# Kernel tuning notes

Measured on AMD Instinct MI355X. Metric: run time of the kernel, lower is better.

## Reference

```python
import jax, jax.numpy as jnp
import numpy as np

NINP = 768
HEAD = 12
ATTN_DIM = 768
PROT_DIM = 1024
B, T, S = 4, 2048, 512
EPS = 1e-5


def _lin_params(key, d_in, d_out):
    k1, k2 = jax.random.split(key)
    lim = 1.0 / np.sqrt(d_in)
    W = jax.random.uniform(k1, (d_in, d_out), jnp.float32, -lim, lim)
    b = jax.random.uniform(k2, (d_out,), jnp.float32, -lim, lim)
    return W, b


def setup_inputs() -> dict:
    key = jax.random.key(0)
    ks = jax.random.split(key, 16)
    x = jax.random.normal(ks[0], (B, T, NINP), jnp.float32)
    enc = jax.random.normal(ks[1], (B, S, PROT_DIM), jnp.float32)
    sWq, sbq = _lin_params(ks[2], NINP, ATTN_DIM)
    sWk, sbk = _lin_params(ks[3], NINP, ATTN_DIM)
    sWv, sbv = _lin_params(ks[4], NINP, ATTN_DIM)
    sWo, sbo = _lin_params(ks[5], ATTN_DIM, NINP)
    cWq, cbq = _lin_params(ks[6], NINP, ATTN_DIM)
    cWk, cbk = _lin_params(ks[7], PROT_DIM, ATTN_DIM)
    cWv, cbv = _lin_params(ks[8], PROT_DIM, ATTN_DIM)
    cWo, cbo = _lin_params(ks[9], ATTN_DIM, NINP)
    mW1, mb1 = _lin_params(ks[10], NINP, 4 * NINP)
    mW2, mb2 = _lin_params(ks[11], 4 * NINP, NINP)
    return dict(
        x=x, encoder_hidden_states=enc,
        ln1_g=jnp.ones((NINP,)), ln1_b=jnp.zeros((NINP,)),
        ln2_g=jnp.ones((NINP,)), ln2_b=jnp.zeros((NINP,)),
        sWq=sWq, sbq=sbq, sWk=sWk, sbk=sbk, sWv=sWv, sbv=sbv, sWo=sWo, sbo=sbo,
        cWq=cWq, cbq=cbq, cWk=cWk, cbk=cbk, cWv=cWv, cbv=cbv, cWo=cWo, cbo=cbo,
        mW1=mW1, mb1=mb1, mW2=mW2, mb2=mb2,
    )


def _ln(x, g, b):
    mu = jnp.mean(x, -1, keepdims=True)
    var = jnp.mean(jnp.square(x - mu), -1, keepdims=True)
    return (x - mu) * jax.lax.rsqrt(var + EPS) * g + b


def _attn(xq, xkv, Wq, bq, Wk, bk, Wv, bv, Wo, bo, causal):
    Bq, Tq, _ = xq.shape
    Sk = xkv.shape[1]
    hd = ATTN_DIM // HEAD
    q = (xq @ Wq + bq).reshape(Bq, Tq, HEAD, hd).transpose(0, 2, 1, 3)
    k = (xkv @ Wk + bk).reshape(Bq, Sk, HEAD, hd).transpose(0, 2, 1, 3)
    v = (xkv @ Wv + bv).reshape(Bq, Sk, HEAD, hd).transpose(0, 2, 1, 3)
    att = jnp.einsum('bhtd,bhsd->bhts', q, k) * (1.0 / np.sqrt(hd))
    if causal:
        mask = jnp.tril(jnp.ones((Tq, Sk), bool))
        att = jnp.where(mask, att, -jnp.inf)
    att = jax.nn.softmax(att, axis=-1)
    y = jnp.einsum('bhts,bhsd->bhtd', att, v)
    y = y.transpose(0, 2, 1, 3).reshape(Bq, Tq, ATTN_DIM)
    return y @ Wo + bo


def reference(x, encoder_hidden_states, ln1_g, ln1_b, ln2_g, ln2_b,
              sWq, sbq, sWk, sbk, sWv, sbv, sWo, sbo,
              cWq, cbq, cWk, cbk, cWv, cbv, cWo, cbo,
              mW1, mb1, mW2, mb2):
    # NOTE: original code does x = ln1(x), so the residual adds onto the
    # NORMED input (faithful to source quirk). is_causal=True, multi_mode=True.
    xn = _ln(x, ln1_g, ln1_b)
    x = xn + _attn(xn, xn, sWq, sbq, sWk, sbk, sWv, sbv, sWo, sbo, causal=True)
    x = x + _attn(x, encoder_hidden_states, cWq, cbq, cWk, cbk, cWv, cbv, cWo, cbo, causal=False)
    h = _ln(x, ln2_g, ln2_b)
    h = jax.nn.gelu(h @ mW1 + mb1, approximate=False) @ mW2 + mb2
    return x + h
```

## Files before the change

kernel.cpp:

```cpp
#include <hip/hip_runtime.h>
#include <math.h>

typedef unsigned short u16;
typedef unsigned int u32;
typedef __attribute__((ext_vector_type(8))) short short8;
typedef __attribute__((ext_vector_type(4))) short bf16x4;
typedef __attribute__((ext_vector_type(2))) unsigned int u32x2;
typedef __attribute__((ext_vector_type(4))) float f32x4;

static __device__ __forceinline__ u16 f2bf(float f) {
    union { float f; unsigned int u; } c; c.f = f;
    unsigned int u = c.u;
    u += 0x7FFF + ((u >> 16) & 1);
    return (u16)(u >> 16);
}
static __device__ __forceinline__ float bf2f(u16 u) {
    union { unsigned int i; float f; } c; c.i = ((unsigned int)u) << 16;
    return c.f;
}
static __device__ __forceinline__ u32 pk2bf(float lo, float hi) {
    u32 r;
    asm("v_cvt_pk_bf16_f32 %0, %1, %2" : "=v"(r) : "v"(lo), "v"(hi));
    return r;
}
static __device__ __forceinline__ float gelu_f(float v) {
    float y = 0.7978845608f * (v + 0.044715f * v * v * v);
    return v / (1.0f + __expf(-2.0f * y));
}

#define GLOAD16(g, s) __builtin_amdgcn_global_load_lds( \
    (const __attribute__((address_space(1))) void*)(g), \
    (__attribute__((address_space(3))) void*)(s), 16, 0, 0)

struct PrepArgs {
    const float* src[11];
    u16* dst[11];
    int K[11];
    int N[11];
    int end[11];
    int cnt;
};

__global__ void k_prep(PrepArgs a)
{
    __shared__ float tile[32][33];
    const int bid = blockIdx.x;
    int e = 0;
    while (e < a.cnt - 1 && bid >= a.end[e]) e++;
    const int local = bid - (e ? a.end[e - 1] : 0);
    const float* __restrict__ src = a.src[e];
    u16* __restrict__ dst = a.dst[e];
    const int K = a.K[e], N = a.N[e];
    const int tx = threadIdx.x, ty = threadIdx.y;

    if (K == 0) {
        size_t base = (size_t)local * 2048 + (size_t)(ty * 32 + tx) * 8;
        float4 v0 = *(const float4*)(src + base);
        float4 v1 = *(const float4*)(src + base + 4);
        short8 o;
        o[0] = (short)f2bf(v0.x); o[1] = (short)f2bf(v0.y);
        o[2] = (short)f2bf(v0.z); o[3] = (short)f2bf(v0.w);
        o[4] = (short)f2bf(v1.x); o[5] = (short)f2bf(v1.y);
        o[6] = (short)f2bf(v1.z); o[7] = (short)f2bf(v1.w);
        *(short8*)&dst[base] = o;
        return;
    }
    const int nbx = N / 32;
    const int bx = local % nbx, by = local / nbx;
    const int n0 = bx * 32, k0 = by * 32;
#pragma unroll
    for (int i = 0; i < 4; i++)
        tile[ty + i * 8][tx] = src[(size_t)(k0 + ty + i * 8) * N + n0 + tx];
    __syncthreads();
#pragma unroll
    for (int i = 0; i < 4; i++)
        dst[(size_t)(n0 + ty + i * 8) * K + k0 + tx] = f2bf(tile[tx][ty + i * 8]);
}

__global__ __launch_bounds__(256) void k_layernorm(
    const float* __restrict__ x, const float* __restrict__ g, const float* __restrict__ b,
    float* __restrict__ outF, u16* __restrict__ outB)
{
    const int row = blockIdx.x, t = threadIdx.x;
    const float* xr = x + (size_t)row * 768;
    float v[3];
#pragma unroll
    for (int i = 0; i < 3; i++) v[i] = xr[t + i * 256];
    __shared__ float sred[4];
    float s = v[0] + v[1] + v[2];
#pragma unroll
    for (int o = 32; o; o >>= 1) s += __shfl_xor(s, o, 64);
    if ((t & 63) == 0) sred[t >> 6] = s;
    __syncthreads();
    float mu = (sred[0] + sred[1] + sred[2] + sred[3]) * (1.0f / 768.0f);
    __syncthreads();
    float q = 0.f;
#pragma unroll
    for (int i = 0; i < 3; i++) { float d = v[i] - mu; q += d * d; }
#pragma unroll
    for (int o = 32; o; o >>= 1) q += __shfl_xor(q, o, 64);
    if ((t & 63) == 0) sred[t >> 6] = q;
    __syncthreads();
    float var = (sred[0] + sred[1] + sred[2] + sred[3]) * (1.0f / 768.0f);
    float rstd = rsqrtf(var + 1e-5f);
#pragma unroll
    for (int i = 0; i < 3; i++) {
        int c = t + i * 256;
        float y = (v[i] - mu) * rstd * g[c] + b[c];
        if (outF) outF[(size_t)row * 768 + c] = y;
        if (outB) outB[(size_t)row * 768 + c] = f2bf(y);
    }
}

template<int BN>
__global__ __launch_bounds__(256) void k_gemm(
    const u16* __restrict__ A, const u16* __restrict__ Bt,
    const float* __restrict__ b1, const float* __restrict__ b2, const float* __restrict__ b3,
    const float* __restrict__ resid,
    float* __restrict__ outF, u16* __restrict__ outB, u16* __restrict__ outK, u16* __restrict__ outV,
    int M, int N, int K, int do_gelu, int mode, int vT_log)
{
    constexpr int MR = (BN == 128) ? 4 : 2;
    __shared__ u16 As[128 * 64];
    __shared__ u16 Bs[BN * 64];
    const int t = threadIdx.x;
    const int w = t >> 6, l = t & 63;
    const int lr = l & 15, lg = l >> 4;

    const unsigned nwg = gridDim.x * gridDim.y;
    unsigned bid = blockIdx.y * gridDim.x + blockIdx.x;
    bid = (bid & 7) * (nwg >> 3) + (bid >> 3);
    const int m0 = (bid / gridDim.x) * 128, n0 = (bid % gridDim.x) * BN;

    const int wr = (BN == 128) ? ((w >> 1) * 64) : (w * 32);
    const int wc = (BN == 128) ? ((w & 1) * 64) : 0;

    const int srow = t >> 3;
    const int sslot = t & 7;

    f32x4 acc[MR][4] = {};

    for (int k0 = 0; k0 < K; k0 += 64) {
        __syncthreads();
#pragma unroll
        for (int i = 0; i < 4; i++) {
            int row = i * 32 + srow;
            GLOAD16(A + (size_t)(m0 + row) * K + k0 + ((sslot ^ (row & 7)) * 8),
                    &As[i * 2048 + w * 512]);
        }
#pragma unroll
        for (int i = 0; i < BN / 32; i++) {
            int row = i * 32 + srow;
            GLOAD16(Bt + (size_t)(n0 + row) * K + k0 + ((sslot ^ (row & 7)) * 8),
                    &Bs[i * 2048 + w * 512]);
        }
        __syncthreads();
#pragma unroll
        for (int kk = 0; kk < 2; kk++) {
            const int ce = kk * 32 + lg * 8;
            short8 af[MR], bfr[4];
#pragma unroll
            for (int m = 0; m < MR; m++) {
                int row = wr + m * 16 + lr;
                af[m] = *(const short8*)&As[row * 64 + (ce ^ ((row & 7) << 3))];
            }
#pragma unroll
            for (int n = 0; n < 4; n++) {
                int row = wc + n * 16 + lr;
                bfr[n] = *(const short8*)&Bs[row * 64 + (ce ^ ((row & 7) << 3))];
            }
#pragma unroll
            for (int m = 0; m < MR; m++)
#pragma unroll
                for (int n = 0; n < 4; n++)
                    acc[m][n] = __builtin_amdgcn_mfma_f32_16x16x32_bf16(af[m], bfr[n], acc[m][n], 0, 0, 0);
        }
    }

#pragma unroll
    for (int m = 0; m < MR; m++) {
        int row0 = m0 + wr + m * 16 + lg * 4;
#pragma unroll
        for (int n = 0; n < 4; n++) {
            int col = n0 + wc + n * 16 + lr;
            const float* bp = b1; int lc = col; u16* tgt = outB; int vT = 0;
            if (mode == 2) {
                if (col >= 1536)     { bp = b3; lc = col - 1536; tgt = outV; vT = 1; }
                else if (col >= 768) { bp = b2; lc = col - 768;  tgt = outK; }
            } else if (mode == 3) {
                if (col >= 768)      { bp = b3; lc = col - 768;  tgt = outV; vT = 1; }
            }
            float bv = bp[lc];
            float vv[4];
#pragma unroll
            for (int j = 0; j < 4; j++) {
                float v = acc[m][n][j] + bv;
                if (do_gelu) v = gelu_f(v);
                vv[j] = v;
            }
            if (mode == 0) {
#pragma unroll
                for (int j = 0; j < 4; j++) {
                    size_t idx = (size_t)(row0 + j) * N + col;
                    float v = vv[j];
                    if (resid) v += resid[idx];
                    if (outF) outF[idx] = v;
                    if (outB) outB[idx] = f2bf(v);
                }
            } else if (!vT) {
#pragma unroll
                for (int j = 0; j < 4; j++)
                    tgt[(size_t)(row0 + j) * 768 + lc] = f2bf(vv[j]);
            } else {
                int head = lc >> 6, d = lc & 63;
                int bq = row0 >> vT_log, s = row0 & ((1 << vT_log) - 1);
                u32x2 pk;
                pk[0] = pk2bf(vv[0], vv[1]);
                pk[1] = pk2bf(vv[2], vv[3]);
                *(u32x2*)&tgt[((size_t)((bq * 12 + head) * 64 + d) << vT_log) + s] = pk;
            }
        }
    }
}

template<bool CAUSAL>
__global__ __launch_bounds__(256) void k_attn(
    const u16* __restrict__ Q, const u16* __restrict__ K,
    const u16* __restrict__ Vt, u16* __restrict__ Y,
    int Tq, int Skv)
{
    const int bh = blockIdx.x;
    const int b = bh / 12, h = bh % 12;
    const int qt = CAUSAL ? ((int)gridDim.y - 1 - (int)blockIdx.y) : blockIdx.y;
    const int q0 = qt * 128;
    const int t = threadIdx.x, w = t >> 6, l = t & 63;
    const int lr = l & 15, lg = l >> 4;
    const int swz = (lr & 7) << 3;
    const float QSC = 0.125f * 1.44269504088896f;

    const u16* Qb = Q + (size_t)b * Tq * 768 + h * 64;
    const u16* Kb = K + (size_t)b * Skv * 768 + h * 64;
    const u16* Vb = Vt + (size_t)bh * 64 * Skv;

    __shared__ u16 Ks[2][64 * 64];
    __shared__ u16 Vs[2][64 * 64];
    __shared__ u16 Ps[4][32 * 64];

    short8 aq[2][2];
#pragma unroll
    for (int qn = 0; qn < 2; qn++) {
        const u16* qr = Qb + (size_t)(q0 + w * 32 + qn * 16 + lr) * 768 + lg * 8;
#pragma unroll
        for (int hh = 0; hh < 2; hh++) {
            short8 raw = *(const short8*)(qr + hh * 32);
            short8 sc;
#pragma unroll
            for (int i = 0; i < 8; i++) sc[i] = (short)f2bf(bf2f((u16)raw[i]) * QSC);
            aq[qn][hh] = sc;
        }
    }

    f32x4 acc[2][4] = {};
    float mrun[2] = { -INFINITY, -INFINITY };
    float lrun[2] = { 0.f, 0.f };

    const int nt = CAUSAL ? (2 * qt + 2) : (Skv / 64);

    const int r0 = t >> 3, r1 = 32 + (t >> 3);
    const int db = (t & 7) * 8;
    const int sw0 = db ^ ((r0 & 7) << 3);
    const int sw1 = db ^ ((r1 & 7) << 3);

    short8 kr0, kr1, vr0, vr1;
    kr0 = *(const short8*)(Kb + (size_t)r0 * 768 + db);
    kr1 = *(const short8*)(Kb + (size_t)r1 * 768 + db);
    vr0 = *(const short8*)(Vb + (size_t)r0 * Skv + db);
    vr1 = *(const short8*)(Vb + (size_t)r1 * Skv + db);
    *(short8*)&Ks[0][r0 * 64 + sw0] = kr0;
    *(short8*)&Ks[0][r1 * 64 + sw1] = kr1;
    *(short8*)&Vs[0][r0 * 64 + sw0] = vr0;
    *(short8*)&Vs[0][r1 * 64 + sw1] = vr1;
    __syncthreads();
    int cur = 0;

    for (int kt = 0; kt < nt; kt++) {
        const int kv0 = kt * 64;
        const bool more = (kt + 1 < nt);
        if (more) {
            const int kn = kv0 + 64;
            kr0 = *(const short8*)(Kb + (size_t)(kn + r0) * 768 + db);
            kr1 = *(const short8*)(Kb + (size_t)(kn + r1) * 768 + db);
            vr0 = *(const short8*)(Vb + (size_t)r0 * Skv + kn + db);
            vr1 = *(const short8*)(Vb + (size_t)r1 * Skv + kn + db);
        }

        const u16* KsC = Ks[cur];
        f32x4 st[2][4];
        __builtin_amdgcn_s_setprio(1);
#pragma unroll
        for (int c = 0; c < 4; c++) {
            const short8 kb0 = *(const short8*)&KsC[(c * 16 + lr) * 64 + ((lg * 8) ^ swz)];
            const short8 kb1 = *(const short8*)&KsC[(c * 16 + lr) * 64 + ((32 | (lg * 8)) ^ swz)];
#pragma unroll
            for (int qn = 0; qn < 2; qn++) {
                f32x4 a = {};
                a = __builtin_amdgcn_mfma_f32_16x16x32_bf16(kb0, aq[qn][0], a, 0, 0, 0);
                a = __builtin_amdgcn_mfma_f32_16x16x32_bf16(kb1, aq[qn][1], a, 0, 0, 0);
                st[qn][c] = a;
            }
        }
        __builtin_amdgcn_s_setprio(0);

        if (CAUSAL && kt >= nt - 2) {
#pragma unroll
            for (int qn = 0; qn < 2; qn++) {
                int qv = q0 + w * 32 + qn * 16 + lr;
#pragma unroll
                for (int c = 0; c < 4; c++)
#pragma unroll
                    for (int j = 0; j < 4; j++) {
                        int kvv = kv0 + c * 16 + lg * 4 + j;
                        if (kvv > qv) st[qn][c][j] = -1e30f;
                    }
            }
        }

        float mv[2];
#pragma unroll
        for (int qn = 0; qn < 2; qn++) {
            float mc[4];
#pragma unroll
            for (int c = 0; c < 4; c++)
                mc[c] = fmaxf(fmaxf(st[qn][c][0], st[qn][c][1]),
                              fmaxf(st[qn][c][2], st[qn][c][3]));
            float m = fmaxf(fmaxf(mc[0], mc[1]), fmaxf(mc[2], mc[3]));
            m = fmaxf(m, __shfl_xor(m, 16, 64));
            m = fmaxf(m, __shfl_xor(m, 32, 64));
            mv[qn] = m;
        }
        float need = fmaxf(mv[0] - mrun[0], mv[1] - mrun[1]);
        if (!__all(need <= 8.0f)) {
#pragma unroll
            for (int qn = 0; qn < 2; qn++) {
                float mnew = fmaxf(mrun[qn], mv[qn]);
                float sc = exp2f(mrun[qn] - mnew);
                mrun[qn] = mnew;
                lrun[qn] *= sc;
#pragma unroll
                for (int c = 0; c < 4; c++)
#pragma unroll
                    for (int j = 0; j < 4; j++) acc[qn][c][j] *= sc;
            }
        }
        u16* pw = Ps[w];
#pragma unroll
        for (int qn = 0; qn < 2; qn++) {
            float rc[4];
            const int prow = qn * 16 + lr;
#pragma unroll
            for (int c = 0; c < 4; c++) {
                float p0 = exp2f(st[qn][c][0] - mrun[qn]);
                float p1 = exp2f(st[qn][c][1] - mrun[qn]);
                float p2 = exp2f(st[qn][c][2] - mrun[qn]);
                float p3 = exp2f(st[qn][c][3] - mrun[qn]);
                rc[c] = (p0 + p1) + (p2 + p3);
                u32x2 pk;
                pk[0] = pk2bf(p0, p1);
                pk[1] = pk2bf(p2, p3);
                *(u32x2*)&pw[prow * 64 + ((c * 16 + lg * 4) ^ swz)] = pk;
            }
            float r = (rc[0] + rc[1]) + (rc[2] + rc[3]);
            r += __shfl_xor(r, 16, 64);
            r += __shfl_xor(r, 32, 64);
            lrun[qn] += r;
        }

        const u16* VsC = Vs[cur];
        __builtin_amdgcn_s_setprio(1);
#pragma unroll
        for (int qn = 0; qn < 2; qn++) {
            const short8 pb0 = *(const short8*)&pw[(qn * 16 + lr) * 64 + ((lg * 8) ^ swz)];
            const short8 pb1 = *(const short8*)&pw[(qn * 16 + lr) * 64 + ((32 | (lg * 8)) ^ swz)];
#pragma unroll
            for (int c = 0; c < 4; c++) {
                const short8 vb0 = *(const short8*)&VsC[(c * 16 + lr) * 64 + ((lg * 8) ^ swz)];
                const short8 vb1 = *(const short8*)&VsC[(c * 16 + lr) * 64 + ((32 | (lg * 8)) ^ swz)];
                acc[qn][c] = __builtin_amdgcn_mfma_f32_16x16x32_bf16(vb0, pb0, acc[qn][c], 0, 0, 0);
                acc[qn][c] = __builtin_amdgcn_mfma_f32_16x16x32_bf16(vb1, pb1, acc[qn][c], 0, 0, 0);
            }
        }
        __builtin_amdgcn_s_setprio(0);

        if (more) {
            *(short8*)&Ks[cur ^ 1][r0 * 64 + sw0] = kr0;
            *(short8*)&Ks[cur ^ 1][r1 * 64 + sw1] = kr1;
            *(short8*)&Vs[cur ^ 1][r0 * 64 + sw0] = vr0;
            *(short8*)&Vs[cur ^ 1][r1 * 64 + sw1] = vr1;
            __syncthreads();
            cur ^= 1;
        }
    }

#pragma unroll
    for (int qn = 0; qn < 2; qn++) {
        float inv = 1.0f / lrun[qn];
        int q = q0 + w * 32 + qn * 16 + lr;
        size_t yb = (size_t)(b * Tq + q) * 768 + h * 64;
#pragma unroll
        for (int c = 0; c < 4; c++) {
            u32x2 pk;
            pk[0] = pk2bf(acc[qn][c][0] * inv, acc[qn][c][1] * inv);
            pk[1] = pk2bf(acc[qn][c][2] * inv, acc[qn][c][3] * inv);
            *(u32x2*)&Y[yb + c * 16 + lg * 4] = pk;
        }
    }
}

extern "C" void kernel_launch(void* const* d_in, const int* in_sizes, int n_in,
                              void* d_out, int out_size, void* d_ws, size_t ws_size,
                              hipStream_t stream)
{
    (void)in_sizes; (void)n_in; (void)out_size; (void)ws_size;
    const float* x    = (const float*)d_in[0];
    const float* enc  = (const float*)d_in[1];
    const float* ln1g = (const float*)d_in[2];
    const float* ln1b = (const float*)d_in[3];
    const float* ln2g = (const float*)d_in[4];
    const float* ln2b = (const float*)d_in[5];
    const float* sWq  = (const float*)d_in[6];
    const float* sbq  = (const float*)d_in[7];
    const float* sWk  = (const float*)d_in[8];
    const float* sbk  = (const float*)d_in[9];
    const float* sWv  = (const float*)d_in[10];
    const float* sbv  = (const float*)d_in[11];
    const float* sWo  = (const float*)d_in[12];
    const float* sbo  = (const float*)d_in[13];
    const float* cWq  = (const float*)d_in[14];
    const float* cbq  = (const float*)d_in[15];
    const float* cWk  = (const float*)d_in[16];
    const float* cbk  = (const float*)d_in[17];
    const float* cWv  = (const float*)d_in[18];
    const float* cbv  = (const float*)d_in[19];
    const float* cWo  = (const float*)d_in[20];
    const float* cbo  = (const float*)d_in[21];
    const float* mW1  = (const float*)d_in[22];
    const float* mb1  = (const float*)d_in[23];
    const float* mW2  = (const float*)d_in[24];
    const float* mb2  = (const float*)d_in[25];
    float* out = (float*)d_out;

    const int Bb = 4, T = 2048, S = 512, C = 768, P = 1024, F = 3072;
    const int M = Bb * T;
    const int MS = Bb * S;

    char* ws = (char*)d_ws;
    size_t off = 0;
    auto alloc = [&](size_t bytes) -> void* {
        void* p = ws + off;
        off += (bytes + 255) & ~(size_t)255;
        return p;
    };

    u16* wqkvT = (u16*)alloc((size_t)3 * C * C * 2);
    u16* sWoT  = (u16*)alloc((size_t)C * C * 2);
    u16* cWqT  = (u16*)alloc((size_t)C * C * 2);
    u16* ckvT  = (u16*)alloc((size_t)2 * C * P * 2);
    u16* cWoT  = (u16*)alloc((size_t)C * C * 2);
    u16* mW1T  = (u16*)alloc((size_t)F * C * 2);
    u16* mW2T  = (u16*)alloc((size_t)C * F * 2);
    u16* encbf = (u16*)alloc((size_t)MS * P * 2);
    float* slotA = (float*)alloc((size_t)M * C * 4);
    float* slotB = (float*)alloc((size_t)M * C * 4);
    u16*   slotC = (u16*)alloc((size_t)M * C * 2);
    u16*   big   = (u16*)alloc((size_t)M * F * 2);

    u16* qbf = big;
    u16* kbf = big + (size_t)M * C;
    u16* vbf = big + (size_t)2 * M * C;
    u16* ybf = big + (size_t)3 * M * C;
    u16* midbf = big;

    float* xn = slotA;
    float* x2 = slotA;
    float* x1 = slotB;
    u16* xbf = slotC;

    PrepArgs pa;
    const float* srcs[11] = { sWq, sWk, sWv, sWo, cWq, cWk, cWv, cWo, mW1, mW2, enc };
    u16* dsts[11] = { wqkvT, wqkvT + (size_t)C * C, wqkvT + (size_t)2 * C * C,
                      sWoT, cWqT, ckvT, ckvT + (size_t)C * P, cWoT, mW1T, mW2T, encbf };
    int Ks_[11] = { C, C, C, C, C, P, P, C, C, F, 0 };
    int Ns_[11] = { C, C, C, C, C, C, C, C, F, C, MS * P };
    int cum = 0;
    for (int i = 0; i < 11; i++) {
        pa.src[i] = srcs[i]; pa.dst[i] = dsts[i]; pa.K[i] = Ks_[i]; pa.N[i] = Ns_[i];
        int nb = Ks_[i] ? (Ns_[i] / 32) * (Ks_[i] / 32) : (Ns_[i] / 2048);
        cum += nb; pa.end[i] = cum;
    }
    pa.cnt = 11;
    k_prep<<<cum, dim3(32, 8), 0, stream>>>(pa);

    k_layernorm<<<M, 256, 0, stream>>>(x, ln1g, ln1b, xn, xbf);

    k_gemm<128><<<dim3(18, 64), 256, 0, stream>>>(
        xbf, wqkvT, sbq, sbk, sbv, nullptr, nullptr, qbf, kbf, vbf, M, 2304, C, 0, 2, 11);

    k_attn<true><<<dim3(Bb * 12, T / 128), 256, 0, stream>>>(qbf, kbf, vbf, ybf, T, T);

    k_gemm<64><<<dim3(12, 64), 256, 0, stream>>>(
        ybf, sWoT, sbo, nullptr, nullptr, xn, x1, xbf, nullptr, nullptr, M, C, C, 0, 0, 0);

    k_gemm<64><<<dim3(12, 64), 256, 0, stream>>>(
        xbf, cWqT, cbq, nullptr, nullptr, nullptr, nullptr, qbf, nullptr, nullptr, M, C, C, 0, 0, 0);

    k_gemm<64><<<dim3(24, 16), 256, 0, stream>>>(
        encbf, ckvT, cbk, nullptr, cbv, nullptr, nullptr, kbf, nullptr, vbf, MS, 1536, P, 0, 3, 9);

    k_attn<false><<<dim3(Bb * 12, T / 128), 256, 0, stream>>>(qbf, kbf, vbf, ybf, T, S);

    k_gemm<64><<<dim3(12, 64), 256, 0, stream>>>(
        ybf, cWoT, cbo, nullptr, nullptr, x1, x2, nullptr, nullptr, nullptr, M, C, C, 0, 0, 0);

    k_layernorm<<<M, 256, 0, stream>>>(x2, ln2g, ln2b, nullptr, xbf);

    k_gemm<128><<<dim3(24, 64), 256, 0, stream>>>(
        xbf, mW1T, mb1, nullptr, nullptr, nullptr, nullptr, midbf, nullptr, nullptr, M, F, C, 1, 0, 0);

    k_gemm<64><<<dim3(12, 64), 256, 0, stream>>>(
        midbf, mW2T, mb2, nullptr, nullptr, x2, out, nullptr, nullptr, nullptr, M, C, F, 0, 0, 0);
}
```

Measured before the change: 425.0 us.

## Use 256-row GEMM tiles for N=768 GEMMs and defer attention row reductions

Adds a BM template parameter to the GEMM so the four N=768 projections use 256x64 tiles (384 blocks instead of 768). Each wave then owns 64 rows, which increases reuse of the B tile. In attention, the cross-lane max shuffles now run only on the rescale path, and the row-sum shuffles move out of the KV loop into the epilogue. Q scaling now uses packed bf16 conversion. Fewer, larger GEMM blocks may underfill the GPU's CUs, and the rescale check now uses each lane's local max rather than the full row max.

Measured after the change: 489.1 us. +15.1%, slower.

```diff
diff --git a/kernel.cpp b/kernel.cpp
--- a/kernel.cpp
+++ b/kernel.cpp
@@ -4,7 +4,6 @@
 typedef unsigned short u16;
 typedef unsigned int u32;
 typedef __attribute__((ext_vector_type(8))) short short8;
-typedef __attribute__((ext_vector_type(4))) short bf16x4;
 typedef __attribute__((ext_vector_type(2))) unsigned int u32x2;
 typedef __attribute__((ext_vector_type(4))) float f32x4;
 
@@ -112,7 +111,7 @@
     }
 }
 
-template<int BN>
+template<int BM, int BN>
 __global__ __launch_bounds__(256) void k_gemm(
     const u16* __restrict__ A, const u16* __restrict__ Bt,
     const float* __restrict__ b1, const float* __restrict__ b2, const float* __restrict__ b3,
@@ -120,8 +119,8 @@
     float* __restrict__ outF, u16* __restrict__ outB, u16* __restrict__ outK, u16* __restrict__ outV,
     int M, int N, int K, int do_gelu, int mode, int vT_log)
 {
-    constexpr int MR = (BN == 128) ? 4 : 2;
-    __shared__ u16 As[128 * 64];
+    constexpr int MR = (BM == 256 || BN == 128) ? 4 : 2;
+    __shared__ u16 As[BM * 64];
     __shared__ u16 Bs[BN * 64];
     const int t = threadIdx.x;
     const int w = t >> 6, l = t & 63;
@@ -130,9 +129,9 @@
     const unsigned nwg = gridDim.x * gridDim.y;
     unsigned bid = blockIdx.y * gridDim.x + blockIdx.x;
     bid = (bid & 7) * (nwg >> 3) + (bid >> 3);
-    const int m0 = (bid / gridDim.x) * 128, n0 = (bid % gridDim.x) * BN;
-
-    const int wr = (BN == 128) ? ((w >> 1) * 64) : (w * 32);
+    const int m0 = (bid / gridDim.x) * BM, n0 = (bid % gridDim.x) * BN;
+
+    const int wr = (BM == 256) ? (w * 64) : ((BN == 128) ? ((w >> 1) * 64) : (w * 32));
     const int wc = (BN == 128) ? ((w & 1) * 64) : 0;
 
     const int srow = t >> 3;
@@ -143,7 +142,7 @@
     for (int k0 = 0; k0 < K; k0 += 64) {
         __syncthreads();
 #pragma unroll
-        for (int i = 0; i < 4; i++) {
+        for (int i = 0; i < BM / 32; i++) {
             int row = i * 32 + srow;
             GLOAD16(A + (size_t)(m0 + row) * K + k0 + ((sslot ^ (row & 7)) * 8),
                     &As[i * 2048 + w * 512]);
@@ -253,10 +252,11 @@
 #pragma unroll
         for (int hh = 0; hh < 2; hh++) {
             short8 raw = *(const short8*)(qr + hh * 32);
-            short8 sc;
-#pragma unroll
-            for (int i = 0; i < 8; i++) sc[i] = (short)f2bf(bf2f((u16)raw[i]) * QSC);
-            aq[qn][hh] = sc;
+            union { short8 s; u32 u[4]; } cv;
+#pragma unroll
+            for (int i = 0; i < 4; i++)
+                cv.u[i] = pk2bf(bf2f((u16)raw[2 * i]) * QSC, bf2f((u16)raw[2 * i + 1]) * QSC);
+            aq[qn][hh] = cv.s;
         }
     }
 
@@ -325,7 +325,7 @@
             }
         }
 
-        float mv[2];
+        float lmax[2];
 #pragma unroll
         for (int qn = 0; qn < 2; qn++) {
             float mc[4];
@@ -333,16 +333,16 @@
             for (int c = 0; c < 4; c++)
                 mc[c] = fmaxf(fmaxf(st[qn][c][0], st[qn][c][1]),
                               fmaxf(st[qn][c][2], st[qn][c][3]));
-            float m = fmaxf(fmaxf(mc[0], mc[1]), fmaxf(mc[2], mc[3]));
-            m = fmaxf(m, __shfl_xor(m, 16, 64));
-            m = fmaxf(m, __shfl_xor(m, 32, 64));
-            mv[qn] = m;
-        }
-        float need = fmaxf(mv[0] - mrun[0], mv[1] - mrun[1]);
+            lmax[qn] = fmaxf(fmaxf(mc[0], mc[1]), fmaxf(mc[2], mc[3]));
+        }
+        float need = fmaxf(lmax[0] - mrun[0], lmax[1] - mrun[1]);
         if (!__all(need <= 8.0f)) {
 #pragma unroll
             for (int qn = 0; qn < 2; qn++) {
-                float mnew = fmaxf(mrun[qn], mv[qn]);
+                float m = lmax[qn];
+                m = fmaxf(m, __shfl_xor(m, 16, 64));
+                m = fmaxf(m, __shfl_xor(m, 32, 64));
+                float mnew = fmaxf(mrun[qn], m);
                 float sc = exp2f(mrun[qn] - mnew);
                 mrun[qn] = mnew;
                 lrun[qn] *= sc;
@@ -369,10 +369,7 @@
                 pk[1] = pk2bf(p2, p3);
                 *(u32x2*)&pw[prow * 64 + ((c * 16 + lg * 4) ^ swz)] = pk;
             }
-            float r = (rc[0] + rc[1]) + (rc[2] + rc[3]);
-            r += __shfl_xor(r, 16, 64);
-            r += __shfl_xor(r, 32, 64);
-            lrun[qn] += r;
+            lrun[qn] += (rc[0] + rc[1]) + (rc[2] + rc[3]);
         }
 
         const u16* VsC = Vs[cur];
@@ -403,7 +400,10 @@
 
 #pragma unroll
     for (int qn = 0; qn < 2; qn++) {
-        float inv = 1.0f / lrun[qn];
+        float tot = lrun[qn];
+        tot += __shfl_xor(tot, 16, 64);
+        tot += __shfl_xor(tot, 32, 64);
+        float inv = 1.0f / tot;
         int q = q0 + w * 32 + qn * 16 + lr;
         size_t yb = (size_t)(b * Tq + q) * 768 + h * 64;
 #pragma unroll
@@ -502,30 +502,30 @@
 
     k_layernorm<<<M, 256, 0, stream>>>(x, ln1g, ln1b, xn, xbf);
 
-    k_gemm<128><<<dim3(18, 64), 256, 0, stream>>>(
+    k_gemm<128, 128><<<dim3(18, 64), 256, 0, stream>>>(
         xbf, wqkvT, sbq, sbk, sbv, nullptr, nullptr, qbf, kbf, vbf, M, 2304, C, 0, 2, 11);
 
     k_attn<true><<<dim3(Bb * 12, T / 128), 256, 0, stream>>>(qbf, kbf, vbf, ybf, T, T);
 
-    k_gemm<64><<<dim3(12, 64), 256, 0, stream>>>(
+    k_gemm<256, 64><<<dim3(12, 32), 256, 0, stream>>>(
         ybf, sWoT, sbo, nullptr, nullptr, xn, x1, xbf, nullptr, nullptr, M, C, C, 0, 0, 0);
 
-    k_gemm<64><<<dim3(12, 64), 256, 0, stream>>>(
+    k_gemm<256, 64><<<dim3(12, 32), 256, 0, stream>>>(
         xbf, cWqT, cbq, nullptr, nullptr, nullptr, nullptr, qbf, nullptr, nullptr, M, C, C, 0, 0, 0);
 
-    k_gemm<64><<<dim3(24, 16), 256, 0, stream>>>(
+    k_gemm<128, 64><<<dim3(24, 16), 256, 0, stream>>>(
         encbf, ckvT, cbk, nullptr, cbv, nullptr, nullptr, kbf, nullptr, vbf, MS, 1536, P, 0, 3, 9);
 
     k_attn<false><<<dim3(Bb * 12, T / 128), 256, 0, stream>>>(qbf, kbf, vbf, ybf, T, S);
 
-    k_gemm<64><<<dim3(12, 64), 256, 0, stream>>>(
+    k_gemm<256, 64><<<dim3(12, 32), 256, 0, stream>>>(
         ybf, cWoT, cbo, nullptr, nullptr, x1, x2, nullptr, nullptr, nullptr, M, C, C, 0, 0, 0);
 
     k_layernorm<<<M, 256, 0, stream>>>(x2, ln2g, ln2b, nullptr, xbf);
 
-    k_gemm<128><<<dim3(24, 64), 256, 0, stream>>>(
+    k_gemm<128, 128><<<dim3(24, 64), 256, 0, stream>>>(
         xbf, mW1T, mb1, nullptr, nullptr, nullptr, nullptr, midbf, nullptr, nullptr, M, F, C, 1, 0, 0);
 
-    k_gemm<64><<<dim3(12, 64), 256, 0, stream>>>(
+    k_gemm<256, 64><<<dim3(12, 32), 256, 0, stream>>>(
         midbf, mW2T, mb2, nullptr, nullptr, x2, out, nullptr, nullptr, nullptr, M, C, F, 0, 0, 0);
 }
```
